# Performance work log

Measured on AMD Instinct MI355X. Metric: run time of the kernel, lower is better.

The kernel has to match this reference:

```python
import jax, jax.numpy as jnp
import numpy as np

MARGIN_TRIPLE = 0.2
MARGIN_INTER = 0.1
SQUARED = False


def _pairwise_distances(embs, squared):
    # Standard stable euclidean pairwise distances.
    dot = embs @ embs.T                      # (B, B)
    sq = jnp.diag(dot)                       # (B,)
    d = jnp.maximum(sq[None, :] - 2.0 * dot + sq[:, None], 0.0)
    if not squared:
        zero = (d == 0.0).astype(d.dtype)
        d = jnp.sqrt(d + zero * 1e-16) * (1.0 - zero)
    return d


def setup_inputs() -> dict:
    key = jax.random.key(0)
    k1, k2 = jax.random.split(key)
    embs = jax.random.normal(k1, (96, 512), dtype=jnp.float32)
    idtys = jax.random.randint(k2, (96,), 0, 16, dtype=jnp.int64)
    return {"embs": embs, "idtys": idtys}


def reference(embs, idtys):
    B = idtys.shape[0]
    d = _pairwise_distances(embs, SQUARED)          # (B, B)

    eq = idtys[None, :] == idtys[:, None]            # (B, B) same-identity
    ne = ~eq
    not_eye = ~jnp.eye(B, dtype=bool)

    # --- batch-hard triplet mining ---
    mask_ap = (not_eye & eq).astype(d.dtype)
    ap_dist = mask_ap * d
    hardest_pos = jnp.max(ap_dist, axis=1, keepdims=True)      # (B, 1)
    pos_ind = jnp.argmax(ap_dist, axis=1, keepdims=True)       # (B, 1)

    mask_an = ne.astype(d.dtype)
    max_d = jnp.max(d, axis=1, keepdims=True)
    an_dist = d + max_d * (1.0 - mask_an)
    hardest_neg = jnp.min(an_dist, axis=1, keepdims=True)      # (B, 1)
    neg_ind = jnp.argmin(an_dist, axis=1, keepdims=True)       # (B, 1)

    triplet_loss = jax.nn.relu(hardest_pos - hardest_neg + MARGIN_TRIPLE)  # (B, 1)

    # --- quadruplet mask: (i!=j) & (y_i==y_j) & (y_j!=y_k) & (y_k!=y_l) & (y_i!=y_l) ---
    qmask = (not_eye[:, :, None, None]
             & eq[:, :, None, None]
             & ne[None, :, :, None]
             & ne[None, None, :, :]
             & ne[:, None, None, :])                            # (B, B, B, B)

    # O(B^4) inter-class loss tensor, as in the original module
    icl = jax.nn.relu(d[:, :, None, None] - d[None, None, :, :] + MARGIN_INTER) * qmask.astype(d.dtype)

    # advanced indexing: indices broadcast (B,), (B,1), (B,1) -> (B, B); result (B, B, B)
    sel = icl[jnp.arange(B), pos_ind, neg_ind]
    inter_class_loss = jnp.max(sel, axis=1, keepdims=True)      # (B, 1, B)

    # (B,1) + (B,1,B) broadcasts to (B,B,B), then mean -> scalar
    return jnp.mean(triplet_loss + inter_class_loss)
```

## Files before the change

### kernel.cpp

```cpp
#include <hip/hip_runtime.h>
#include <math.h>

#define B 96
#define D 512
#define DPAD 97
#define MARGIN_TRIPLE 0.2f
#define MARGIN_INTER  0.1f

__global__ __launch_bounds__(256)
void bhq_dots(const float* __restrict__ embs, float* __restrict__ dot) {
    __shared__ float ei[D];
    const int i   = blockIdx.x;
    const int tid = threadIdx.x;
    for (int k = tid; k < D; k += 256) ei[k] = embs[i * D + k];
    __syncthreads();
    const int wave = tid >> 6;
    const int lane = tid & 63;
    for (int j = wave; j < B; j += 4) {
        const float* ej = embs + j * D;
        float s = 0.f;
#pragma unroll
        for (int m = 0; m < D / 64; ++m) {
            const int k = lane + m * 64;
            s += ei[k] * ej[k];
        }
#pragma unroll
        for (int off = 32; off > 0; off >>= 1) s += __shfl_xor(s, off, 64);
        if (lane == 0) dot[i * B + j] = s;
    }
}

__global__ __launch_bounds__(256)
void bhq_mine(const float* __restrict__ dot, const int* __restrict__ idty,
              float* __restrict__ out) {
    __shared__ float ds[B][DPAD];
    __shared__ float sq[B];
    __shared__ int   y[B];
    __shared__ float hp_s[B], hn_s[B];
    __shared__ int   p_s[B], n_s[B], haspos_s[B];
    __shared__ float wsum[4];

    const int tid = threadIdx.x;
    if (tid < B) {
        sq[tid] = dot[tid * B + tid];
        y[tid]  = idty[tid];
    }
    __syncthreads();

    for (int idx = tid; idx < B * B; idx += 256) {
        const int i = idx / B, j = idx - i * B;
        float v = sq[i] - 2.f * dot[idx] + sq[j];
        v = fmaxf(v, 0.f);
        ds[i][j] = (v == 0.f) ? 0.f : sqrtf(v);
    }
    __syncthreads();

    if (tid < B) {
        const int r  = tid;
        const int yr = y[r];
        float maxd = -INFINITY;
        for (int j = 0; j < B; ++j) maxd = fmaxf(maxd, ds[r][j]);

        float hp = -INFINITY; int p = 0; int haspos = 0;
        for (int j = 0; j < B; ++j) {
            const bool pos = (j != r) && (y[j] == yr);
            haspos |= (int)pos;
            const float ap = pos ? ds[r][j] : 0.f;
            if (ap > hp) { hp = ap; p = j; }
        }
        float hn = INFINITY; int n = 0;
        for (int j = 0; j < B; ++j) {
            const float an = ds[r][j] + ((y[j] == yr) ? maxd : 0.f);
            if (an < hn) { hn = an; n = j; }
        }
        hp_s[r] = hp; hn_s[r] = hn; p_s[r] = p; n_s[r] = n; haspos_s[r] = haspos;
    }
    __syncthreads();

    float tloc = 0.f;
    if (tid < B) tloc = fmaxf(hp_s[tid] - hn_s[tid] + MARGIN_TRIPLE, 0.f);

    float iloc = 0.f;
    for (int idx = tid; idx < B * B; idx += 256) {
        const int x = idx / B, l = idx - x * B;
        const int p = p_s[x], n = n_s[x];
        const int yp = y[p], yn = y[n], yl = y[l];
        if (yp != yn && haspos_s[p] && yl != yp && yl != yn) {
            iloc += fmaxf(hp_s[p] - ds[n][l] + MARGIN_INTER, 0.f);
        }
    }

    float v = tloc * (1.f / B) + iloc * (1.f / (B * B));
#pragma unroll
    for (int off = 32; off > 0; off >>= 1) v += __shfl_xor(v, off, 64);
    if ((tid & 63) == 0) wsum[tid >> 6] = v;
    __syncthreads();
    if (tid == 0) {
        float s = wsum[0] + wsum[1] + wsum[2] + wsum[3];
        out[0] = s;
    }
}

extern "C" void kernel_launch(void* const* d_in, const int* in_sizes, int n_in,
                              void* d_out, int out_size, void* d_ws, size_t ws_size,
                              hipStream_t stream) {
    const float* embs = (const float*)d_in[0];
    const int*   idty = (const int*)d_in[1];
    float*       out  = (float*)d_out;
    float*       dot  = (float*)d_ws;

    bhq_dots<<<B, 256, 0, stream>>>(embs, dot);
    bhq_mine<<<1, 256, 0, stream>>>(dot, idty, out);
}
```

Before: 90.66 us.

## Move distance and hardest-mining per row into parallel blocks

Each of the 96 blocks now computes its own row of distances, recomputing squared norms inline, and mines the hardest positive and negative with wave-level shuffle reductions. This replaces the serial per-thread loops in the single-block second kernel. The final kernel only computes the quadruplet sum from the precomputed per-row results, removing the single-block B×B distance conversion and the serial argmax/argmin scans. In exchange, each block redundantly computes norms of every row, and the final kernel reads distances from global memory instead of shared memory.

```diff
diff --git a/kernel.cpp b/kernel.cpp
--- a/kernel.cpp
+++ b/kernel.cpp
@@ -3,102 +3,146 @@
 
 #define B 96
 #define D 512
-#define DPAD 97
 #define MARGIN_TRIPLE 0.2f
 #define MARGIN_INTER  0.1f
 
 __global__ __launch_bounds__(256)
-void bhq_dots(const float* __restrict__ embs, float* __restrict__ dot) {
+void bhq_rows(const float* __restrict__ embs, const int* __restrict__ idty,
+              float* __restrict__ wsD, float* __restrict__ wsHP,
+              float* __restrict__ wsHN, int* __restrict__ wsP,
+              int* __restrict__ wsN, int* __restrict__ wsHas) {
     __shared__ float ei[D];
-    const int i   = blockIdx.x;
-    const int tid = threadIdx.x;
-    for (int k = tid; k < D; k += 256) ei[k] = embs[i * D + k];
-    __syncthreads();
+    __shared__ float drow[B];
+    __shared__ int   y[B];
+    __shared__ float ssred[4];
+
+    const int i    = blockIdx.x;
+    const int tid  = threadIdx.x;
     const int wave = tid >> 6;
     const int lane = tid & 63;
+
+    float ss = 0.f;
+    for (int k = tid; k < D; k += 256) {
+        float v = embs[i * D + k];
+        ei[k] = v;
+        ss += v * v;
+    }
+#pragma unroll
+    for (int off = 32; off > 0; off >>= 1) ss += __shfl_xor(ss, off, 64);
+    if (lane == 0) ssred[wave] = ss;
+    if (tid < B) y[tid] = idty[tid];
+    __syncthreads();
+    const float ssi = ssred[0] + ssred[1] + ssred[2] + ssred[3];
+
     for (int j = wave; j < B; j += 4) {
         const float* ej = embs + j * D;
-        float s = 0.f;
+        float s = 0.f, s2 = 0.f;
 #pragma unroll
         for (int m = 0; m < D / 64; ++m) {
-            const int k = lane + m * 64;
-            s += ei[k] * ej[k];
+            float a = ei[lane + m * 64];
+            float b = ej[lane + m * 64];
+            s  += a * b;
+            s2 += b * b;
         }
 #pragma unroll
-        for (int off = 32; off > 0; off >>= 1) s += __shfl_xor(s, off, 64);
-        if (lane == 0) dot[i * B + j] = s;
+        for (int off = 32; off > 0; off >>= 1) {
+            s  += __shfl_xor(s,  off, 64);
+            s2 += __shfl_xor(s2, off, 64);
+        }
+        if (lane == 0) {
+            float v = fmaxf(ssi + s2 - 2.f * s, 0.f);
+            drow[j] = (j == i || v == 0.f) ? 0.f : sqrtf(v);
+        }
     }
+    __syncthreads();
+
+    if (wave == 0) {
+        const int  yr   = y[i];
+        const int  j0   = lane, j1 = lane + 64;
+        const bool has1 = (lane < 32);
+        const float d0 = drow[j0];
+        const float d1 = has1 ? drow[j1] : 0.f;
+        const int   y0 = y[j0];
+        const int   y1 = has1 ? y[j1] : -1;
+
+        float mx = fmaxf(d0, has1 ? d1 : -INFINITY);
+#pragma unroll
+        for (int off = 32; off > 0; off >>= 1) mx = fmaxf(mx, __shfl_xor(mx, off, 64));
+
+        const bool pos0 = (j0 != i) && (y0 == yr);
+        const bool pos1 = has1 && (j1 != i) && (y1 == yr);
+        float a0 = pos0 ? d0 : 0.f;
+        float a1 = has1 ? (pos1 ? d1 : 0.f) : -INFINITY;
+        float bv; int bi;
+        if (a1 > a0) { bv = a1; bi = j1; } else { bv = a0; bi = j0; }
+#pragma unroll
+        for (int off = 32; off > 0; off >>= 1) {
+            float ov = __shfl_xor(bv, off, 64);
+            int   oi = __shfl_xor(bi, off, 64);
+            if (ov > bv || (ov == bv && oi < bi)) { bv = ov; bi = oi; }
+        }
+
+        float n0 = d0 + ((y0 == yr) ? mx : 0.f);
+        float n1 = has1 ? (d1 + ((y1 == yr) ? mx : 0.f)) : INFINITY;
+        float cv; int ci;
+        if (n1 < n0) { cv = n1; ci = j1; } else { cv = n0; ci = j0; }
+#pragma unroll
+        for (int off = 32; off > 0; off >>= 1) {
+            float ov = __shfl_xor(cv, off, 64);
+            int   oi = __shfl_xor(ci, off, 64);
+            if (ov < cv || (ov == cv && oi < ci)) { cv = ov; ci = oi; }
+        }
+
+        unsigned long long bal = __ballot(pos0 || pos1);
+        if (lane == 0) {
+            wsHP[i]  = bv;
+            wsHN[i]  = cv;
+            wsP[i]   = bi;
+            wsN[i]   = ci;
+            wsHas[i] = (bal != 0ULL) ? 1 : 0;
+        }
+    }
+    if (tid < B) wsD[i * B + tid] = drow[tid];
 }
 
 __global__ __launch_bounds__(256)
-void bhq_mine(const float* __restrict__ dot, const int* __restrict__ idty,
-              float* __restrict__ out) {
-    __shared__ float ds[B][DPAD];
-    __shared__ float sq[B];
-    __shared__ int   y[B];
-    __shared__ float hp_s[B], hn_s[B];
-    __shared__ int   p_s[B], n_s[B], haspos_s[B];
+void bhq_final(const float* __restrict__ wsD, const float* __restrict__ wsHP,
+               const float* __restrict__ wsHN, const int* __restrict__ wsP,
+               const int* __restrict__ wsN, const int* __restrict__ wsHas,
+               const int* __restrict__ idty, float* __restrict__ out) {
+    __shared__ float hp[B], hn[B];
+    __shared__ int   p[B], n[B], has[B], y[B];
     __shared__ float wsum[4];
-
     const int tid = threadIdx.x;
     if (tid < B) {
-        sq[tid] = dot[tid * B + tid];
-        y[tid]  = idty[tid];
+        hp[tid]  = wsHP[tid];
+        hn[tid]  = wsHN[tid];
+        p[tid]   = wsP[tid];
+        n[tid]   = wsN[tid];
+        has[tid] = wsHas[tid];
+        y[tid]   = idty[tid];
     }
     __syncthreads();
 
-    for (int idx = tid; idx < B * B; idx += 256) {
-        const int i = idx / B, j = idx - i * B;
-        float v = sq[i] - 2.f * dot[idx] + sq[j];
-        v = fmaxf(v, 0.f);
-        ds[i][j] = (v == 0.f) ? 0.f : sqrtf(v);
-    }
-    __syncthreads();
+    float acc = 0.f;
+    if (tid < B) acc = fmaxf(hp[tid] - hn[tid] + MARGIN_TRIPLE, 0.f) * (1.f / B);
 
-    if (tid < B) {
-        const int r  = tid;
-        const int yr = y[r];
-        float maxd = -INFINITY;
-        for (int j = 0; j < B; ++j) maxd = fmaxf(maxd, ds[r][j]);
-
-        float hp = -INFINITY; int p = 0; int haspos = 0;
-        for (int j = 0; j < B; ++j) {
-            const bool pos = (j != r) && (y[j] == yr);
-            haspos |= (int)pos;
-            const float ap = pos ? ds[r][j] : 0.f;
-            if (ap > hp) { hp = ap; p = j; }
-        }
-        float hn = INFINITY; int n = 0;
-        for (int j = 0; j < B; ++j) {
-            const float an = ds[r][j] + ((y[j] == yr) ? maxd : 0.f);
-            if (an < hn) { hn = an; n = j; }
-        }
-        hp_s[r] = hp; hn_s[r] = hn; p_s[r] = p; n_s[r] = n; haspos_s[r] = haspos;
-    }
-    __syncthreads();
-
-    float tloc = 0.f;
-    if (tid < B) tloc = fmaxf(hp_s[tid] - hn_s[tid] + MARGIN_TRIPLE, 0.f);
-
-    float iloc = 0.f;
+    float il = 0.f;
     for (int idx = tid; idx < B * B; idx += 256) {
         const int x = idx / B, l = idx - x * B;
-        const int p = p_s[x], n = n_s[x];
-        const int yp = y[p], yn = y[n], yl = y[l];
-        if (yp != yn && haspos_s[p] && yl != yp && yl != yn) {
-            iloc += fmaxf(hp_s[p] - ds[n][l] + MARGIN_INTER, 0.f);
+        const int px = p[x], nx = n[x];
+        const int yp = y[px], yn = y[nx], yl = y[l];
+        if (yp != yn && has[px] && yl != yp && yl != yn) {
+            il += fmaxf(hp[px] - wsD[nx * B + l] + MARGIN_INTER, 0.f);
         }
     }
+    acc += il * (1.f / (B * B));
 
-    float v = tloc * (1.f / B) + iloc * (1.f / (B * B));
 #pragma unroll
-    for (int off = 32; off > 0; off >>= 1) v += __shfl_xor(v, off, 64);
-    if ((tid & 63) == 0) wsum[tid >> 6] = v;
+    for (int off = 32; off > 0; off >>= 1) acc += __shfl_xor(acc, off, 64);
+    if ((tid & 63) == 0) wsum[tid >> 6] = acc;
     __syncthreads();
-    if (tid == 0) {
-        float s = wsum[0] + wsum[1] + wsum[2] + wsum[3];
-        out[0] = s;
-    }
+    if (tid == 0) out[0] = wsum[0] + wsum[1] + wsum[2] + wsum[3];
 }
 
 extern "C" void kernel_launch(void* const* d_in, const int* in_sizes, int n_in,
@@ -107,8 +151,14 @@
     const float* embs = (const float*)d_in[0];
     const int*   idty = (const int*)d_in[1];
     float*       out  = (float*)d_out;
-    float*       dot  = (float*)d_ws;
 
-    bhq_dots<<<B, 256, 0, stream>>>(embs, dot);
-    bhq_mine<<<1, 256, 0, stream>>>(dot, idty, out);
+    float* wsD   = (float*)d_ws;
+    float* wsHP  = wsD + B * B;
+    float* wsHN  = wsHP + B;
+    int*   wsP   = (int*)(wsHN + B);
+    int*   wsN   = wsP + B;
+    int*   wsHas = wsN + B;
+
+    bhq_rows<<<B, 256, 0, stream>>>(embs, idty, wsD, wsHP, wsHN, wsP, wsN, wsHas);
+    bhq_final<<<1, 256, 0, stream>>>(wsD, wsHP, wsHN, wsP, wsN, wsHas, idty, out);
 }
```

Result: faster. 83.84 us (-7.5%).
